# Kernel tuning notes

Hardware: AMD Instinct MI355X
Metric: run time of the kernel (lower is better)

The kernel has to match this reference:

```python
import jax, jax.numpy as jnp
import numpy as np

N = 131072      # total sentences
D = 512         # d_MLP_size == bag_feature_dim
D_ATT = 256
N_HEAD = 4
N_CLASSES = 53
BAG_SIZE = 16
N_BAGS = N // BAG_SIZE


def setup_inputs() -> dict:
    key = jax.random.key(0)
    k_x, k_w1, k_w2, k_wc, k_bc = jax.random.split(key, 5)
    x = jax.random.normal(k_x, (N, D), dtype=jnp.float32)
    # equal-sized bags (ragged boundaries collapsed to segment ids)
    seg_ids = (jnp.arange(N, dtype=jnp.int32) // BAG_SIZE).astype(jnp.int32)
    # parameters, stored (in, out); math identical to nn.Linear(x @ W.T)
    W1 = jax.random.normal(k_w1, (D, D_ATT), dtype=jnp.float32) / np.sqrt(D)
    W2 = jax.random.normal(k_w2, (D_ATT, N_HEAD), dtype=jnp.float32) / np.sqrt(D_ATT)
    Wc = jax.random.normal(k_wc, (D, N_CLASSES), dtype=jnp.float32) / np.sqrt(D)
    bc = jax.random.normal(k_bc, (N_CLASSES,), dtype=jnp.float32) * 0.01
    return {"x": x, "W1": W1, "W2": W2, "Wc": Wc, "bc": bc,
            "seg_ids": seg_ids, "n_bags": N_BAGS}


def reference(x, W1, W2, Wc, bc, seg_ids, n_bags):
    # scores per sentence per head: tanh(x W1) W2  -> (N, H)
    s = jnp.tanh(x @ W1) @ W2
    # segment-wise (per-bag) softmax over sentences, per head
    smax = jax.ops.segment_max(s, seg_ids, num_segments=n_bags)      # (B, H)
    e = jnp.exp(s - smax[seg_ids])                                   # (N, H)
    denom = jax.ops.segment_sum(e, seg_ids, num_segments=n_bags)     # (B, H)
    alpha = e / denom[seg_ids]                                       # (N, H)
    # torch: mean over heads of (H, n_i) attention, then alpha @ x
    w = jnp.mean(alpha, axis=1)                                      # (N,)
    bag_repr = jax.ops.segment_sum(w[:, None] * x, seg_ids,
                                   num_segments=n_bags)              # (B, D)
    # dropout is identity in eval / p=0
    logits = bag_repr @ Wc + bc                                      # (B, C)
    return logits
```

## Files before the change

kernel.cpp:

```cpp
#include <hip/hip_runtime.h>
#include <hip/hip_bf16.h>

#define N_TOTAL   131072
#define D         512
#define D_ATT     256
#define N_HEAD    4
#define N_CLASSES 53
#define BAG       16
#define M_TILE    128
#define BK        64
#define BAGS_PER_BLK (M_TILE / BAG)
#define THREADS   512
#define N_BLOCKS  (N_TOTAL / M_TILE)

typedef __attribute__((ext_vector_type(8))) short bf16x8;
typedef __attribute__((ext_vector_type(4))) float f32x4;

__device__ __forceinline__ unsigned short f2bf(float f) {
    __hip_bfloat16 h = __float2bfloat16(f);
    return *reinterpret_cast<unsigned short*>(&h);
}
__device__ __forceinline__ float bfbits2f(unsigned int lo16) {
    unsigned int v = lo16 << 16;
    return __uint_as_float(v);
}
__device__ __forceinline__ float bfhi2f(unsigned int hibits) {
    return __uint_as_float(hibits & 0xffff0000u);
}

__global__ void prep_kernel(const float* __restrict__ W1, const float* __restrict__ Wc,
                            unsigned short* __restrict__ W1T, float* __restrict__ WcT) {
    int tid = blockIdx.x * 256 + threadIdx.x;
    if (tid < D * D_ATT) {
        int k = tid >> 8;
        int n = tid & 255;
        W1T[n * D + k] = f2bf(W1[k * D_ATT + n]);
    } else {
        int t2 = tid - D * D_ATT;
        if (t2 < D * N_CLASSES) {
            int k = t2 / N_CLASSES;
            int c = t2 - k * N_CLASSES;
            WcT[c * D + k] = Wc[k * N_CLASSES + c];
        }
    }
}

#define LDA 72
#define LDB 72
#define LDH 258
#define LDR 516

__global__ void __launch_bounds__(THREADS)
fused_kernel(const float* __restrict__ x,
             const unsigned short* __restrict__ W1T,
             const float* __restrict__ W2,
             const float* __restrict__ WcT,
             const float* __restrict__ bc,
             float* __restrict__ out)
{
    __shared__ __align__(16) unsigned char lds_u[66048];
    __shared__ float ldsW2T[N_HEAD * D_ATT];
    __shared__ float ldsS[M_TILE * N_HEAD];
    __shared__ float ldsM[BAGS_PER_BLK * N_HEAD];
    __shared__ float ldsDen[BAGS_PER_BLK * N_HEAD];
    __shared__ float ldsW[M_TILE];

    unsigned short* ldsA = (unsigned short*)lds_u;
    unsigned short* ldsB = (unsigned short*)(lds_u + 18432);
    unsigned short* ldsH = (unsigned short*)lds_u;
    float*          ldsR = (float*)lds_u;

    const int tid  = threadIdx.x;
    const int wave = tid >> 6;
    const int lane = tid & 63;
    const int quad = lane >> 4;
    const int l16  = lane & 15;
    const int wr   = (wave & 1) * 64;
    const int wc2  = (wave >> 1) * 64;
    const int row_base = blockIdx.x * M_TILE;

    for (int i = tid; i < D_ATT * N_HEAD; i += THREADS) {
        int n = i >> 2, h = i & 3;
        ldsW2T[h * D_ATT + n] = W2[i];
    }

    f32x4 acc[4][4] = {};

    for (int kt = 0; kt < D / BK; ++kt) {
        #pragma unroll
        for (int i = 0; i < 4; ++i) {
            int f  = i * THREADS + tid;
            int r  = f >> 4;
            int kc = (f & 15) << 2;
            const float4 v = *reinterpret_cast<const float4*>(
                &x[(size_t)(row_base + r) * D + kt * BK + kc]);
            unsigned int p0 = (unsigned int)f2bf(v.x) | ((unsigned int)f2bf(v.y) << 16);
            unsigned int p1 = (unsigned int)f2bf(v.z) | ((unsigned int)f2bf(v.w) << 16);
            uint2 p; p.x = p0; p.y = p1;
            *reinterpret_cast<uint2*>(&ldsA[r * LDA + kc]) = p;
        }
        #pragma unroll
        for (int i = 0; i < 4; ++i) {
            int cdx = i * THREADS + tid;
            int r   = cdx >> 3;
            int kc  = (cdx & 7) << 3;
            uint4 v = *reinterpret_cast<const uint4*>(&W1T[(size_t)r * D + kt * BK + kc]);
            *reinterpret_cast<uint4*>(&ldsB[r * LDB + kc]) = v;
        }
        __syncthreads();

        #pragma unroll
        for (int kk = 0; kk < 2; ++kk) {
            const int kb = kk * 32 + quad * 8;
            bf16x8 af[4], bfr[4];
            #pragma unroll
            for (int mi = 0; mi < 4; ++mi)
                af[mi] = *reinterpret_cast<const bf16x8*>(&ldsA[(wr + mi * 16 + l16) * LDA + kb]);
            #pragma unroll
            for (int ni = 0; ni < 4; ++ni)
                bfr[ni] = *reinterpret_cast<const bf16x8*>(&ldsB[(wc2 + ni * 16 + l16) * LDB + kb]);
            #pragma unroll
            for (int mi = 0; mi < 4; ++mi)
                #pragma unroll
                for (int ni = 0; ni < 4; ++ni)
                    acc[mi][ni] = __builtin_amdgcn_mfma_f32_16x16x32_bf16(
                        af[mi], bfr[ni], acc[mi][ni], 0, 0, 0);
        }
        __syncthreads();
    }

    #pragma unroll
    for (int mi = 0; mi < 4; ++mi) {
        #pragma unroll
        for (int ni = 0; ni < 4; ++ni) {
            f32x4 v = acc[mi][ni];
            #pragma unroll
            for (int r = 0; r < 4; ++r) {
                float e = __expf(2.f * v[r]);
                float t = 1.f - 2.f / (e + 1.f);
                int row = wr + mi * 16 + quad * 4 + r;
                int col = wc2 + ni * 16 + l16;
                ldsH[row * LDH + col] = f2bf(t);
            }
        }
    }
    __syncthreads();

    {
        const int row  = tid >> 2;
        const int head = tid & 3;
        const unsigned short* hrow = &ldsH[row * LDH];
        const float* w2h = &ldsW2T[head * D_ATT];
        float s = 0.f;
        #pragma unroll 8
        for (int j = 0; j < 64; ++j) {
            uint2 u = *reinterpret_cast<const uint2*>(&hrow[j * 4]);
            float4 wv = *reinterpret_cast<const float4*>(&w2h[j * 4]);
            s += bfbits2f(u.x & 0xffffu) * wv.x + bfhi2f(u.x) * wv.y
               + bfbits2f(u.y & 0xffffu) * wv.z + bfhi2f(u.y) * wv.w;
        }
        ldsS[row * 4 + head] = s;
    }
    __syncthreads();

    if (tid < BAGS_PER_BLK * N_HEAD) {
        int bag = tid >> 2, head = tid & 3;
        float m = -1e30f;
        for (int i = 0; i < BAG; ++i)
            m = fmaxf(m, ldsS[(bag * BAG + i) * 4 + head]);
        float den = 0.f;
        for (int i = 0; i < BAG; ++i)
            den += __expf(ldsS[(bag * BAG + i) * 4 + head] - m);
        ldsM[tid] = m;
        ldsDen[tid] = 1.f / den;
    }
    __syncthreads();
    if (tid < M_TILE) {
        int row = tid, bag = row >> 4;
        float w = 0.f;
        #pragma unroll
        for (int h = 0; h < 4; ++h)
            w += __expf(ldsS[row * 4 + h] - ldsM[bag * 4 + h]) * ldsDen[bag * 4 + h];
        ldsW[row] = 0.25f * w;
    }
    __syncthreads();

    {
        const int b  = tid >> 6;
        const int dc = (tid & 63) * 8;
        float4 r0 = {0.f, 0.f, 0.f, 0.f}, r1 = {0.f, 0.f, 0.f, 0.f};
        for (int i = 0; i < BAG; ++i) {
            int row = b * BAG + i;
            float wv = ldsW[row];
            const float4* xp = reinterpret_cast<const float4*>(
                &x[(size_t)(row_base + row) * D + dc]);
            float4 a = xp[0], c = xp[1];
            r0.x += wv * a.x; r0.y += wv * a.y; r0.z += wv * a.z; r0.w += wv * a.w;
            r1.x += wv * c.x; r1.y += wv * c.y; r1.z += wv * c.z; r1.w += wv * c.w;
        }
        *reinterpret_cast<float4*>(&ldsR[b * LDR + dc])     = r0;
        *reinterpret_cast<float4*>(&ldsR[b * LDR + dc + 4]) = r1;
    }
    __syncthreads();

    if (tid < 448) {
        int c = tid >> 3;
        int b = tid & 7;
        if (c < N_CLASSES) {
            float a = bc[c];
            const float4* rp = reinterpret_cast<const float4*>(&ldsR[b * LDR]);
            const float4* wp = reinterpret_cast<const float4*>(&WcT[(size_t)c * D]);
            #pragma unroll 8
            for (int j = 0; j < D / 4; ++j) {
                float4 r = rp[j], w = wp[j];
                a += r.x * w.x + r.y * w.y + r.z * w.z + r.w * w.w;
            }
            out[((size_t)blockIdx.x * BAGS_PER_BLK + b) * N_CLASSES + c] = a;
        }
    }
}

extern "C" void kernel_launch(void* const* d_in, const int* in_sizes, int n_in,
                              void* d_out, int out_size, void* d_ws, size_t ws_size,
                              hipStream_t stream) {
    const float* x  = (const float*)d_in[0];
    const float* W1 = (const float*)d_in[1];
    const float* W2 = (const float*)d_in[2];
    const float* Wc = (const float*)d_in[3];
    const float* bc = (const float*)d_in[4];

    unsigned short* W1T = (unsigned short*)d_ws;
    float*          WcT = (float*)((char*)d_ws + (size_t)D * D_ATT * 2);

    int prep_total = D * D_ATT + D * N_CLASSES;
    prep_kernel<<<dim3((prep_total + 255) / 256), dim3(256), 0, stream>>>(W1, Wc, W1T, WcT);

    fused_kernel<<<dim3(N_BLOCKS), dim3(THREADS), 0, stream>>>(
        x, W1T, W2, WcT, bc, (float*)d_out);
}
```

Before: 480.2 us.

## Stage full x tile in LDS and stream W1 fragments directly from global

Halves the row tile to 64 rows and 256 threads, loads the whole 64x512 x tile into LDS once as bf16, and removes the per-k-step LDS staging of W1. Each wave reads its W1T column fragments directly from global/L2 with a register double-buffered software pipeline, so the main loop no longer needs per-iteration barriers. The cost is redundant W1 traffic from every block (now twice as many blocks), scattered 16-byte global loads feeding the MFMAs, and lower MFMA reuse per block.

```diff
diff --git a/kernel.cpp b/kernel.cpp
--- a/kernel.cpp
+++ b/kernel.cpp
@@ -7,10 +7,9 @@
 #define N_HEAD    4
 #define N_CLASSES 53
 #define BAG       16
-#define M_TILE    128
-#define BK        64
+#define M_TILE    64
 #define BAGS_PER_BLK (M_TILE / BAG)
-#define THREADS   512
+#define THREADS   256
 #define N_BLOCKS  (N_TOTAL / M_TILE)
 
 typedef __attribute__((ext_vector_type(8))) short bf16x8;
@@ -21,8 +20,7 @@
     return *reinterpret_cast<unsigned short*>(&h);
 }
 __device__ __forceinline__ float bfbits2f(unsigned int lo16) {
-    unsigned int v = lo16 << 16;
-    return __uint_as_float(v);
+    return __uint_as_float(lo16 << 16);
 }
 __device__ __forceinline__ float bfhi2f(unsigned int hibits) {
     return __uint_as_float(hibits & 0xffff0000u);
@@ -45,9 +43,8 @@
     }
 }
 
-#define LDA 72
-#define LDB 72
-#define LDH 258
+#define LDX 520
+#define LDH 260
 #define LDR 516
 
 __global__ void __launch_bounds__(THREADS)
@@ -58,25 +55,23 @@
              const float* __restrict__ bc,
              float* __restrict__ out)
 {
-    __shared__ __align__(16) unsigned char lds_u[66048];
+    __shared__ __align__(16) unsigned char lds_u[66560];
     __shared__ float ldsW2T[N_HEAD * D_ATT];
     __shared__ float ldsS[M_TILE * N_HEAD];
     __shared__ float ldsM[BAGS_PER_BLK * N_HEAD];
     __shared__ float ldsDen[BAGS_PER_BLK * N_HEAD];
     __shared__ float ldsW[M_TILE];
 
-    unsigned short* ldsA = (unsigned short*)lds_u;
-    unsigned short* ldsB = (unsigned short*)(lds_u + 18432);
+    unsigned short* ldsX = (unsigned short*)lds_u;
     unsigned short* ldsH = (unsigned short*)lds_u;
-    float*          ldsR = (float*)lds_u;
+    float*          ldsR = (float*)(lds_u + 33280);
 
     const int tid  = threadIdx.x;
     const int wave = tid >> 6;
     const int lane = tid & 63;
     const int quad = lane >> 4;
     const int l16  = lane & 15;
-    const int wr   = (wave & 1) * 64;
-    const int wc2  = (wave >> 1) * 64;
+    const int wc2  = wave * 64;
     const int row_base = blockIdx.x * M_TILE;
 
     for (int i = tid; i < D_ATT * N_HEAD; i += THREADS) {
@@ -84,50 +79,60 @@
         ldsW2T[h * D_ATT + n] = W2[i];
     }
 
-    f32x4 acc[4][4] = {};
-
-    for (int kt = 0; kt < D / BK; ++kt) {
-        #pragma unroll
-        for (int i = 0; i < 4; ++i) {
+    {
+        const float* xb = &x[(size_t)row_base * D];
+        #pragma unroll 8
+        for (int i = 0; i < 32; ++i) {
             int f  = i * THREADS + tid;
-            int r  = f >> 4;
-            int kc = (f & 15) << 2;
-            const float4 v = *reinterpret_cast<const float4*>(
-                &x[(size_t)(row_base + r) * D + kt * BK + kc]);
+            int r  = f >> 7;
+            int c4 = f & 127;
+            float4 v = *reinterpret_cast<const float4*>(&xb[(size_t)r * D + c4 * 4]);
             unsigned int p0 = (unsigned int)f2bf(v.x) | ((unsigned int)f2bf(v.y) << 16);
             unsigned int p1 = (unsigned int)f2bf(v.z) | ((unsigned int)f2bf(v.w) << 16);
             uint2 p; p.x = p0; p.y = p1;
-            *reinterpret_cast<uint2*>(&ldsA[r * LDA + kc]) = p;
-        }
+            *reinterpret_cast<uint2*>(&ldsX[r * LDX + c4 * 4]) = p;
+        }
+    }
+    __syncthreads();
+
+    f32x4 acc[4][4] = {};
+    {
+        const unsigned short* Wb = &W1T[(size_t)wc2 * D];
+        bf16x8 a0[4], b0[4], a1[4], b1[4];
+
+        #define LOAD_A(ks, dst)                                                        \
+            { int kb = (ks) * 32 + quad * 8;                                           \
+              _Pragma("unroll")                                                        \
+              for (int mi = 0; mi < 4; ++mi)                                           \
+                  dst[mi] = *reinterpret_cast<const bf16x8*>(                          \
+                      &ldsX[(mi * 16 + l16) * LDX + kb]); }
+        #define LOAD_B(ks, dst)                                                        \
+            { int kb = (ks) * 32 + quad * 8;                                           \
+              _Pragma("unroll")                                                        \
+              for (int ni = 0; ni < 4; ++ni)                                           \
+                  dst[ni] = *reinterpret_cast<const bf16x8*>(                          \
+                      &Wb[(size_t)(ni * 16 + l16) * D + kb]); }
+        #define MFMA(af, bfr)                                                          \
+            { _Pragma("unroll")                                                        \
+              for (int mi = 0; mi < 4; ++mi)                                           \
+                  _Pragma("unroll")                                                    \
+                  for (int ni = 0; ni < 4; ++ni)                                       \
+                      acc[mi][ni] = __builtin_amdgcn_mfma_f32_16x16x32_bf16(           \
+                          af[mi], bfr[ni], acc[mi][ni], 0, 0, 0); }
+
+        LOAD_A(0, a0); LOAD_B(0, b0);
         #pragma unroll
-        for (int i = 0; i < 4; ++i) {
-            int cdx = i * THREADS + tid;
-            int r   = cdx >> 3;
-            int kc  = (cdx & 7) << 3;
-            uint4 v = *reinterpret_cast<const uint4*>(&W1T[(size_t)r * D + kt * BK + kc]);
-            *reinterpret_cast<uint4*>(&ldsB[r * LDB + kc]) = v;
-        }
-        __syncthreads();
-
-        #pragma unroll
-        for (int kk = 0; kk < 2; ++kk) {
-            const int kb = kk * 32 + quad * 8;
-            bf16x8 af[4], bfr[4];
-            #pragma unroll
-            for (int mi = 0; mi < 4; ++mi)
-                af[mi] = *reinterpret_cast<const bf16x8*>(&ldsA[(wr + mi * 16 + l16) * LDA + kb]);
-            #pragma unroll
-            for (int ni = 0; ni < 4; ++ni)
-                bfr[ni] = *reinterpret_cast<const bf16x8*>(&ldsB[(wc2 + ni * 16 + l16) * LDB + kb]);
-            #pragma unroll
-            for (int mi = 0; mi < 4; ++mi)
-                #pragma unroll
-                for (int ni = 0; ni < 4; ++ni)
-                    acc[mi][ni] = __builtin_amdgcn_mfma_f32_16x16x32_bf16(
-                        af[mi], bfr[ni], acc[mi][ni], 0, 0, 0);
-        }
-        __syncthreads();
-    }
+        for (int ks = 0; ks < 16; ks += 2) {
+            LOAD_A(ks + 1, a1); LOAD_B(ks + 1, b1);
+            MFMA(a0, b0);
+            if (ks + 2 < 16) { LOAD_A(ks + 2, a0); LOAD_B(ks + 2, b0); }
+            MFMA(a1, b1);
+        }
+        #undef LOAD_A
+        #undef LOAD_B
+        #undef MFMA
+    }
+    __syncthreads();
 
     #pragma unroll
     for (int mi = 0; mi < 4; ++mi) {
@@ -138,7 +143,7 @@
             for (int r = 0; r < 4; ++r) {
                 float e = __expf(2.f * v[r]);
                 float t = 1.f - 2.f / (e + 1.f);
-                int row = wr + mi * 16 + quad * 4 + r;
+                int row = mi * 16 + quad * 4 + r;
                 int col = wc2 + ni * 16 + l16;
                 ldsH[row * LDH + col] = f2bf(t);
             }
@@ -186,8 +191,8 @@
     __syncthreads();
 
     {
-        const int b  = tid >> 6;
-        const int dc = (tid & 63) * 8;
+        const int b  = wave;
+        const int dc = lane * 8;
         float4 r0 = {0.f, 0.f, 0.f, 0.f}, r1 = {0.f, 0.f, 0.f, 0.f};
         for (int i = 0; i < BAG; ++i) {
             int row = b * BAG + i;
@@ -203,9 +208,9 @@
     }
     __syncthreads();
 
-    if (tid < 448) {
-        int c = tid >> 3;
-        int b = tid & 7;
+    {
+        int c = tid >> 2;
+        int b = tid & 3;
         if (c < N_CLASSES) {
             float a = bc[c];
             const float4* rp = reinterpret_cast<const float4*>(&ldsR[b * LDR]);
```

Result: no change. 476.4 us (-0.8%).
